# Kernel optimization log

Hardware: AMD Instinct MI355X
Metric: run time of the kernel (lower is better)

The kernel has to match this reference:

```python
import jax, jax.numpy as jnp
import numpy as np

N_NODES = 100000
N_EDGES = 1600000
IN_DIM, HID_DIM, OUT_DIM = 128, 64, 1


def setup_inputs() -> dict:
    key = jax.random.key(0)
    ks = jax.random.split(key, 8)
    x = jax.random.normal(ks[0], (N_NODES, IN_DIM), dtype=jnp.float32)
    edge_index = jax.random.randint(ks[1], (2, N_EDGES), 0, N_NODES, dtype=jnp.int64)
    # Glorot-ish scaled weights
    W1 = jax.random.normal(ks[2], (IN_DIM, HID_DIM), dtype=jnp.float32) / np.sqrt(IN_DIM)
    b1 = jnp.zeros((HID_DIM,), dtype=jnp.float32)
    W2 = jax.random.normal(ks[3], (HID_DIM, HID_DIM), dtype=jnp.float32) / np.sqrt(HID_DIM)
    b2 = jnp.zeros((HID_DIM,), dtype=jnp.float32)
    W3 = jax.random.normal(ks[4], (HID_DIM, OUT_DIM), dtype=jnp.float32) / np.sqrt(HID_DIM)
    b3 = jnp.zeros((OUT_DIM,), dtype=jnp.float32)
    return {"x": x, "edge_index": edge_index, "W1": W1, "b1": b1,
            "W2": W2, "b2": b2, "W3": W3, "b3": b3}


def _gcn_norm(edge_index, num_nodes):
    # PyG gcn_norm with add_self_loops=True, edge_weight=1:
    # deg[i] = 1 (self loop) + #incoming edges at i (dst = edge_index[1])
    dst = edge_index[1]
    deg = jnp.ones((num_nodes,), dtype=jnp.float32).at[dst].add(1.0)
    dis = jnp.where(deg > 0, 1.0 / jnp.sqrt(deg), 0.0)  # deg_inv_sqrt
    return dis


def _gcn_conv(x, W, b, src, dst, dis):
    h = x @ W                                   # [N, F_out] transform first (PyG order)
    norm = dis[src] * dis[dst]                  # [E]
    msg = h[src] * norm[:, None]                # gather + scale, [E, F_out]
    out = jnp.zeros_like(h).at[dst].add(msg)    # scatter-add aggregation
    out = out + h * (dis * dis)[:, None]        # self-loop contribution
    return out + b


def reference(x, edge_index, W1, b1, W2, b2, W3, b3):
    src, dst = edge_index[0], edge_index[1]
    dis = _gcn_norm(edge_index, x.shape[0])
    h = jax.nn.relu(_gcn_conv(x, W1, b1, src, dst, dis))   # dropout = identity (eval)
    h = jax.nn.relu(_gcn_conv(h, W2, b2, src, dst, dis))
    return _gcn_conv(h, W3, b3, src, dst, dis)
```

## Files before the change

### kernel.cpp

```cpp
#include <hip/hip_runtime.h>

#define IN_DIM 128
#define HID 64
#define MAXC 400
#define MAXB 512
#define EPB 4096
#define DPT 512
#define G1CAP 6144

static __device__ __forceinline__ unsigned short f2bf(float f) {
    unsigned u = __float_as_uint(f);
    u += 0x7FFF + ((u >> 16) & 1);
    return (unsigned short)(u >> 16);
}

typedef short bf16x8 __attribute__((ext_vector_type(8)));
typedef float f32x4 __attribute__((ext_vector_type(4)));

__global__ __launch_bounds__(256) void k_hist2(const int* __restrict__ dst,
                                               int* __restrict__ hmat, int E, int NC) {
    __shared__ int h[MAXC];
    int tid = threadIdx.x, blk = blockIdx.x;
    for (int i = tid; i < NC; i += 256) h[i] = 0;
    __syncthreads();
    int e0 = blk * EPB, e1 = min(e0 + EPB, E);
    for (int e = e0 + tid; e < e1; e += 256) atomicAdd(&h[dst[e] >> 8], 1);
    __syncthreads();
    for (int i = tid; i < NC; i += 256) hmat[blk * MAXC + i] = h[i];
}

__global__ __launch_bounds__(512) void k_bktscan(int* __restrict__ hmat,
                                                 int* __restrict__ bktTotal,
                                                 int NBLK, int NC) {
    __shared__ int tmp[512];
    int cb = blockIdx.x;
    int t = threadIdx.x;
    int v = (t < NBLK) ? hmat[t * MAXC + cb] : 0;
    tmp[t] = v;
    __syncthreads();
    for (int off = 1; off < 512; off <<= 1) {
        int a = (t >= off) ? tmp[t - off] : 0;
        __syncthreads();
        tmp[t] += a;
        __syncthreads();
    }
    if (t < NBLK) hmat[t * MAXC + cb] = tmp[t] - v;
    if (t == 511) bktTotal[cb] = tmp[511];
}

__global__ __launch_bounds__(512) void k_cscan(const int* __restrict__ bktTotal,
                                               int* __restrict__ coarseStart,
                                               int* __restrict__ rowStart,
                                               int NC, int N, int E) {
    __shared__ int tmp[512];
    int t = threadIdx.x;
    int v = (t < NC) ? bktTotal[t] : 0;
    tmp[t] = v;
    __syncthreads();
    for (int off = 1; off < 512; off <<= 1) {
        int a = (t >= off) ? tmp[t - off] : 0;
        __syncthreads();
        tmp[t] += a;
        __syncthreads();
    }
    int excl = tmp[t] - v;
    if (t < NC) coarseStart[t] = excl;
    if (t == NC - 1) coarseStart[NC] = excl + v;
    if (t == 0) rowStart[N] = E;
}

__global__ __launch_bounds__(256) void k_part1(const int* __restrict__ src,
                                               const int* __restrict__ dst,
                                               const int* __restrict__ hmat,
                                               const int* __restrict__ coarseStart,
                                               int* __restrict__ tmp1,
                                               int E, int NC) {
    __shared__ int bcnt[MAXC];
    __shared__ int bbase[MAXC];
    int tid = threadIdx.x, blk = blockIdx.x;
    for (int i = tid; i < NC; i += 256) {
        bcnt[i] = 0;
        bbase[i] = coarseStart[i] + hmat[blk * MAXC + i];
    }
    __syncthreads();
    int e0 = blk * EPB, e1 = min(e0 + EPB, E);
    for (int e = e0 + tid; e < e1; e += 256) {
        int s = src[e], d = dst[e];
        int cb = d >> 8;
        int slot = bbase[cb] + atomicAdd(&bcnt[cb], 1);
        tmp1[slot] = s | ((d & 255) << 17);
    }
}

__global__ __launch_bounds__(DPT) void k_degplace(const int* __restrict__ tmp1,
                                                  const int* __restrict__ coarseStart,
                                                  float* __restrict__ dis,
                                                  int* __restrict__ rowStart,
                                                  int* __restrict__ esrc, int N) {
    __shared__ int hist[256];
    __shared__ int scn[256];
    __shared__ int cur[256];
    int tid = threadIdx.x;
    int cb = blockIdx.x;
    int node0 = cb << 8;
    const int r0 = coarseStart[cb], r1 = coarseStart[cb + 1];
    if (tid < 256) hist[tid] = 0;
    __syncthreads();
    for (int i = r0 + tid; i < r1; i += DPT)
        atomicAdd(&hist[((unsigned)tmp1[i]) >> 17], 1);
    __syncthreads();
    int v = 0;
    if (tid < 256) { v = hist[tid]; scn[tid] = v; }
    __syncthreads();
    for (int off = 1; off < 256; off <<= 1) {
        int a = 0;
        if (tid < 256 && tid >= off) a = scn[tid - off];
        __syncthreads();
        if (tid < 256) scn[tid] += a;
        __syncthreads();
    }
    if (tid < 256) {
        int myStart = r0 + scn[tid] - v;
        cur[tid] = myStart;
        int node = node0 + tid;
        if (node < N) {
            dis[node] = rsqrtf((float)v + 1.0f);
            rowStart[node] = myStart;
        }
    }
    __syncthreads();
    for (int i = r0 + tid; i < r1; i += DPT) {
        int pk = tmp1[i];
        int dl = ((unsigned)pk) >> 17;
        int pos = atomicAdd(&cur[dl], 1);
        esrc[pos] = (pk & 0x1FFFF) << 7;
    }
}

template <int K, typename T>
__global__ __launch_bounds__(256) void k_mmx(const T* __restrict__ X,
                                             const float* __restrict__ W,
                                             const float* __restrict__ dis,
                                             unsigned short* __restrict__ Hbs, int N) {
    constexpr int WP = K + 8;
    __shared__ unsigned short Wt[64 * WP];
    const int tid = threadIdx.x;
    for (int i = tid; i < K * 64; i += 256) {
        int k = i >> 6, n = i & 63;
        Wt[n * WP + k] = f2bf(W[i]);
    }
    __syncthreads();
    const int lane = tid & 63;
    const int m16 = lane & 15;
    const int quad = lane >> 4;
    const int rowBase = blockIdx.x * 64 + (tid >> 6) * 16;
    const int rowc = min(rowBase + m16, N - 1);

    f32x4 acc0 = {0.f, 0.f, 0.f, 0.f};
    f32x4 acc1 = acc0, acc2 = acc0, acc3 = acc0;
    const T* xrow = X + (size_t)rowc * K;
#pragma unroll
    for (int k0 = 0; k0 < K; k0 += 32) {
        bf16x8 af;
        if constexpr (sizeof(T) == 4) {
            const float* xp = (const float*)xrow + k0 + quad * 8;
            float4 xa = *(const float4*)xp;
            float4 xb = *(const float4*)(xp + 4);
            af[0] = (short)f2bf(xa.x); af[1] = (short)f2bf(xa.y);
            af[2] = (short)f2bf(xa.z); af[3] = (short)f2bf(xa.w);
            af[4] = (short)f2bf(xb.x); af[5] = (short)f2bf(xb.y);
            af[6] = (short)f2bf(xb.z); af[7] = (short)f2bf(xb.w);
        } else {
            af = *(const bf16x8*)((const unsigned short*)xrow + k0 + quad * 8);
        }
        const unsigned short* wp = &Wt[m16 * WP + k0 + quad * 8];
        bf16x8 b0 = *(const bf16x8*)(wp);
        bf16x8 b1 = *(const bf16x8*)(wp + 16 * WP);
        bf16x8 b2 = *(const bf16x8*)(wp + 32 * WP);
        bf16x8 b3 = *(const bf16x8*)(wp + 48 * WP);
        acc0 = __builtin_amdgcn_mfma_f32_16x16x32_bf16(af, b0, acc0, 0, 0, 0);
        acc1 = __builtin_amdgcn_mfma_f32_16x16x32_bf16(af, b1, acc1, 0, 0, 0);
        acc2 = __builtin_amdgcn_mfma_f32_16x16x32_bf16(af, b2, acc2, 0, 0, 0);
        acc3 = __builtin_amdgcn_mfma_f32_16x16x32_bf16(af, b3, acc3, 0, 0, 0);
    }
#pragma unroll
    for (int reg = 0; reg < 4; ++reg) {
        int r = rowBase + quad * 4 + reg;
        if (r < N) {
            float dsc = dis[r];
            unsigned short* hp = Hbs + (size_t)r * 64 + m16;
            hp[0]  = f2bf(acc0[reg] * dsc);
            hp[16] = f2bf(acc1[reg] * dsc);
            hp[32] = f2bf(acc2[reg] * dsc);
            hp[48] = f2bf(acc3[reg] * dsc);
        }
    }
}


#define BLO(d) __uint_as_float((d) << 16)
#define BHI(d) __uint_as_float((d) & 0xFFFF0000u)
#define ACC4(L, H, Q) { L.x += BLO((Q).x); L.y += BHI((Q).x);                  \
                        L.z += BLO((Q).y); L.w += BHI((Q).y);                  \
                        H.x += BLO((Q).z); H.y += BHI((Q).z);                  \
                        H.z += BLO((Q).w); H.w += BHI((Q).w); }

template <int MODE>
__global__ __launch_bounds__(256) void k_gather64(const unsigned short* __restrict__ Hbs,
                                                  const int* __restrict__ esrc,
                                                  const int* __restrict__ rowStart,
                                                  const float* __restrict__ dis,
                                                  const float* __restrict__ b,
                                                  unsigned short* __restrict__ outB,
                                                  const float* __restrict__ W3,
                                                  const float* __restrict__ b3,
                                                  float* __restrict__ colS,
                                                  float* __restrict__ outF,
                                                  int N) {
    int lane = threadIdx.x & 63;
    int c = lane & 7;
    int oct = lane >> 3;
    int ob = oct << 3;
    int wave = (blockIdx.x * 256 + threadIdx.x) >> 6;
    int g0 = wave * 8;
    if (g0 >= N) return;
    const char* hb = (const char*)Hbs + c * 16;

    int rb = rowStart[min(g0 + lane, N)];
    int Rq  = __shfl(rb, oct, 64);
    int Rq1 = __shfl(rb, oct + 1, 64);
    int n = g0 + oct;
    int nc = min(n, N - 1);

    float4 aL, aH;
    {
        uint4 sd = *(const uint4*)(hb + ((size_t)nc << 7));
        aL.x = BLO(sd.x); aL.y = BHI(sd.x); aL.z = BLO(sd.y); aL.w = BHI(sd.y);
        aH.x = BLO(sd.z); aH.y = BHI(sd.z); aH.z = BLO(sd.w); aH.w = BHI(sd.w);
    }

    unsigned eoff = (Rq + c < Rq1) ? (unsigned)esrc[Rq + c] : 0u;
    for (int bb = Rq; bb < Rq1; bb += 8) {
        int cnt = min(8, Rq1 - bb);
        unsigned eoffN = (bb + 8 + c < Rq1) ? (unsigned)esrc[bb + 8 + c] : 0u;

        if (cnt == 8) {
            unsigned o0 = __shfl(eoff, ob + 0, 64);
            unsigned o1 = __shfl(eoff, ob + 1, 64);
            unsigned o2 = __shfl(eoff, ob + 2, 64);
            unsigned o3 = __shfl(eoff, ob + 3, 64);
            unsigned o4 = __shfl(eoff, ob + 4, 64);
            unsigned o5 = __shfl(eoff, ob + 5, 64);
            unsigned o6 = __shfl(eoff, ob + 6, 64);
            unsigned o7 = __shfl(eoff, ob + 7, 64);
            uint4 q0 = *(const uint4*)(hb + o0);
            uint4 q1 = *(const uint4*)(hb + o1);
            uint4 q2 = *(const uint4*)(hb + o2);
            uint4 q3 = *(const uint4*)(hb + o3);
            uint4 q4 = *(const uint4*)(hb + o4);
            uint4 q5 = *(const uint4*)(hb + o5);
            uint4 q6 = *(const uint4*)(hb + o6);
            uint4 q7 = *(const uint4*)(hb + o7);
            ACC4(aL, aH, q0) ACC4(aL, aH, q1) ACC4(aL, aH, q2) ACC4(aL, aH, q3)
            ACC4(aL, aH, q4) ACC4(aL, aH, q5) ACC4(aL, aH, q6) ACC4(aL, aH, q7)
        } else {
            int j = 0;
            if (j + 4 <= cnt) {
                unsigned o0 = __shfl(eoff, ob + j + 0, 64);
                unsigned o1 = __shfl(eoff, ob + j + 1, 64);
                unsigned o2 = __shfl(eoff, ob + j + 2, 64);
                unsigned o3 = __shfl(eoff, ob + j + 3, 64);
                uint4 q0 = *(const uint4*)(hb + o0);
                uint4 q1 = *(const uint4*)(hb + o1);
                uint4 q2 = *(const uint4*)(hb + o2);
                uint4 q3 = *(const uint4*)(hb + o3);
                ACC4(aL, aH, q0) ACC4(aL, aH, q1) ACC4(aL, aH, q2) ACC4(aL, aH, q3)
                j += 4;
            }
            if (j < cnt) {
                bool v1 = j + 1 < cnt, v2 = j + 2 < cnt;
                unsigned o0 = __shfl(eoff, ob + j, 64);
                unsigned o1 = __shfl(eoff, v1 ? ob + j + 1 : ob + j, 64);
                unsigned o2 = __shfl(eoff, v2 ? ob + j + 2 : ob + j, 64);
                uint4 q0 = *(const uint4*)(hb + o0);
                uint4 q1 = *(const uint4*)(hb + o1);
                uint4 q2 = *(const uint4*)(hb + o2);
                if (!v1) { q1.x = q1.y = q1.z = q1.w = 0u; }
                if (!v2) { q2.x = q2.y = q2.z = q2.w = 0u; }
                ACC4(aL, aH, q0) ACC4(aL, aH, q1) ACC4(aL, aH, q2)
            }
        }
        eoff = eoffN;
    }

    float ds = dis[nc];
    float4 bL = ((const float4*)b)[2 * c];
    float4 bH = ((const float4*)b)[2 * c + 1];
    float4 vL, vH;
    vL.x = fmaxf(aL.x * ds + bL.x, 0.f);
    vL.y = fmaxf(aL.y * ds + bL.y, 0.f);
    vL.z = fmaxf(aL.z * ds + bL.z, 0.f);
    vL.w = fmaxf(aL.w * ds + bL.w, 0.f);
    vH.x = fmaxf(aH.x * ds + bH.x, 0.f);
    vH.y = fmaxf(aH.y * ds + bH.y, 0.f);
    vH.z = fmaxf(aH.z * ds + bH.z, 0.f);
    vH.w = fmaxf(aH.w * ds + bH.w, 0.f);

    if (MODE == 1) {
        uint4 pv;
        pv.x = (unsigned)f2bf(vL.x) | ((unsigned)f2bf(vL.y) << 16);
        pv.y = (unsigned)f2bf(vL.z) | ((unsigned)f2bf(vL.w) << 16);
        pv.z = (unsigned)f2bf(vH.x) | ((unsigned)f2bf(vH.y) << 16);
        pv.w = (unsigned)f2bf(vH.z) | ((unsigned)f2bf(vH.w) << 16);
        if (n < N) ((uint4*)outB)[(size_t)n * 8 + c] = pv;
    } else {
        float4 wL = ((const float4*)W3)[2 * c];
        float4 wH = ((const float4*)W3)[2 * c + 1];
        float t = vL.x * wL.x + vL.y * wL.y + vL.z * wL.z + vL.w * wL.w
                + vH.x * wH.x + vH.y * wH.y + vH.z * wH.z + vH.w * wH.w;
        t += __shfl_xor(t, 1, 64);
        t += __shfl_xor(t, 2, 64);
        t += __shfl_xor(t, 4, 64);
        if (c == 0 && n < N) {
            colS[n] = t * ds;
            outF[n] = t * ds * ds + b3[0];
        }
    }
}

__global__ __launch_bounds__(256) void k_gather1(const float* __restrict__ colS,
                                                 const int* __restrict__ esrc,
                                                 const int* __restrict__ rowStart,
                                                 const float* __restrict__ dis,
                                                 float* __restrict__ out, int N) {
    __shared__ float ls[G1CAP];
    int tid = threadIdx.x;
    int n0 = blockIdx.x * 256;
    int nEnd = min(n0 + 256, N);
    int r0 = rowStart[n0];
    int r1 = rowStart[nEnd];
    int cnt = r1 - r0;
    if (cnt <= G1CAP) {
        for (int i = tid; i < cnt; i += 256)
            ls[i] = colS[((unsigned)esrc[r0 + i]) >> 7];
        __syncthreads();
        int n = n0 + tid;
        if (n < N) {
            int a = rowStart[n] - r0, bnd = rowStart[n + 1] - r0;
            float acc = 0.0f;
            for (int e = a; e < bnd; ++e) acc += ls[e];
            out[n] += acc * dis[n];
        }
    } else {
        int n = n0 + tid;
        if (n < N) {
            int a = rowStart[n], bnd = rowStart[n + 1];
            float acc = 0.0f;
            for (int e = a; e < bnd; ++e) acc += colS[((unsigned)esrc[e]) >> 7];
            out[n] += acc * dis[n];
        }
    }
}

extern "C" void kernel_launch(void* const* d_in, const int* in_sizes, int n_in,
                              void* d_out, int out_size, void* d_ws, size_t ws_size,
                              hipStream_t stream) {
    const float* x  = (const float*)d_in[0];
    const int*   ei = (const int*)d_in[1];
    const float* W1 = (const float*)d_in[2];
    const float* b1 = (const float*)d_in[3];
    const float* W2 = (const float*)d_in[4];
    const float* b2 = (const float*)d_in[5];
    const float* W3 = (const float*)d_in[6];
    const float* b3 = (const float*)d_in[7];
    float* out = (float*)d_out;

    const int N = in_sizes[0] / IN_DIM;
    const int E = in_sizes[1] / 2;
    const int* src = ei;
    const int* dst = ei + E;
    const int NC = (N + 255) >> 8;
    const int NBLK = (E + EPB - 1) / EPB;

    char* w = (char*)d_ws;
    auto alloc = [&](size_t bytes) {
        char* p = w;
        w += (bytes + 1023) & ~(size_t)1023;
        return p;
    };
    float*          dis        = (float*)alloc((size_t)N * 4);
    unsigned short* Hbs        = (unsigned short*)alloc((size_t)N * 64 * 2);
    unsigned short* Hb1        = (unsigned short*)alloc((size_t)N * 64 * 2);
    float*          colS       = (float*)alloc((size_t)N * 4);
    int*            rowStart   = (int*)alloc((size_t)(N + 1) * 4);
    int*            bktTotal   = (int*)alloc((size_t)MAXC * 4);
    int*            coarseStart= (int*)alloc((size_t)(MAXC + 1) * 4);
    int*            hmat       = (int*)alloc((size_t)MAXB * MAXC * 4);
    int*            esrc       = (int*)alloc((size_t)E * 4 + 1024);
    int*            tmp1       = (int*)alloc((size_t)E * 4);

    const int NB_N  = (N + 255) / 256;
    const int NB_MX = (N + 63) / 64;
    const int NB_G8 = (((N + 7) / 8) * 64 + 255) / 256;

    k_hist2<<<NBLK, 256, 0, stream>>>(dst, hmat, E, NC);
    k_bktscan<<<NC, 512, 0, stream>>>(hmat, bktTotal, NBLK, NC);
    k_cscan<<<1, 512, 0, stream>>>(bktTotal, coarseStart, rowStart, NC, N, E);
    k_part1<<<NBLK, 256, 0, stream>>>(src, dst, hmat, coarseStart, tmp1, E, NC);
    k_degplace<<<NC, DPT, 0, stream>>>(tmp1, coarseStart, dis, rowStart, esrc, N);

    k_mmx<IN_DIM, float><<<NB_MX, 256, 0, stream>>>(x, W1, dis, Hbs, N);
    k_gather64<1><<<NB_G8, 256, 0, stream>>>(Hbs, esrc, rowStart, dis, b1,
                                             Hb1, nullptr, nullptr, nullptr, nullptr, N);

    k_mmx<HID, unsigned short><<<NB_MX, 256, 0, stream>>>(Hb1, W2, dis, Hbs, N);
    k_gather64<2><<<NB_G8, 256, 0, stream>>>(Hbs, esrc, rowStart, dis, b2,
                                             nullptr, W3, b3, colS, out, N);

    k_gather1<<<NB_N, 256, 0, stream>>>(colS, esrc, rowStart, dis, out, N);
}
```

Baseline: 233.3 us.

## Fuse layer-1 gather with layer-2 matmul and merge scan kernels via last-block

```diff
diff --git a/kernel.cpp b/kernel.cpp
--- a/kernel.cpp
+++ b/kernel.cpp
@@ -18,9 +18,11 @@
 typedef float f32x4 __attribute__((ext_vector_type(4)));
 
 __global__ __launch_bounds__(256) void k_hist2(const int* __restrict__ dst,
-                                               int* __restrict__ hmat, int E, int NC) {
+                                               int* __restrict__ hmat,
+                                               int* __restrict__ ctr, int E, int NC) {
     __shared__ int h[MAXC];
     int tid = threadIdx.x, blk = blockIdx.x;
+    if (blk == 0 && tid == 0) ctr[0] = 0;
     for (int i = tid; i < NC; i += 256) h[i] = 0;
     __syncthreads();
     int e0 = blk * EPB, e1 = min(e0 + EPB, E);
@@ -31,8 +33,12 @@
 
 __global__ __launch_bounds__(512) void k_bktscan(int* __restrict__ hmat,
                                                  int* __restrict__ bktTotal,
-                                                 int NBLK, int NC) {
+                                                 int* __restrict__ ctr,
+                                                 int* __restrict__ coarseStart,
+                                                 int* __restrict__ rowStart,
+                                                 int NBLK, int NC, int N, int E) {
     __shared__ int tmp[512];
+    __shared__ int lastFlag;
     int cb = blockIdx.x;
     int t = threadIdx.x;
     int v = (t < NBLK) ? hmat[t * MAXC + cb] : 0;
@@ -45,17 +51,13 @@
         __syncthreads();
     }
     if (t < NBLK) hmat[t * MAXC + cb] = tmp[t] - v;
-    if (t == 511) bktTotal[cb] = tmp[511];
-}
-
-__global__ __launch_bounds__(512) void k_cscan(const int* __restrict__ bktTotal,
-                                               int* __restrict__ coarseStart,
-                                               int* __restrict__ rowStart,
-                                               int NC, int N, int E) {
-    __shared__ int tmp[512];
-    int t = threadIdx.x;
-    int v = (t < NC) ? bktTotal[t] : 0;
-    tmp[t] = v;
+    if (t == 511) atomicExch(&bktTotal[cb], tmp[511]);
+    __syncthreads();
+    if (t == 0) lastFlag = (atomicAdd(ctr, 1) == (int)gridDim.x - 1);
+    __syncthreads();
+    if (!lastFlag) return;
+    int v2 = (t < NC) ? atomicAdd(&bktTotal[t], 0) : 0;
+    tmp[t] = v2;
     __syncthreads();
     for (int off = 1; off < 512; off <<= 1) {
         int a = (t >= off) ? tmp[t - off] : 0;
@@ -63,9 +65,9 @@
         tmp[t] += a;
         __syncthreads();
     }
-    int excl = tmp[t] - v;
+    int excl = tmp[t] - v2;
     if (t < NC) coarseStart[t] = excl;
-    if (t == NC - 1) coarseStart[NC] = excl + v;
+    if (t == NC - 1) coarseStart[NC] = excl + v2;
     if (t == 0) rowStart[N] = E;
 }
 
@@ -197,7 +199,6 @@
     }
 }
 
-
 #define BLO(d) __uint_as_float((d) << 16)
 #define BHI(d) __uint_as_float((d) & 0xFFFF0000u)
 #define ACC4(L, H, Q) { L.x += BLO((Q).x); L.y += BHI((Q).x);                  \
@@ -205,13 +206,154 @@
                         H.x += BLO((Q).z); H.y += BHI((Q).z);                  \
                         H.z += BLO((Q).w); H.w += BHI((Q).w); }
 
-template <int MODE>
-__global__ __launch_bounds__(256) void k_gather64(const unsigned short* __restrict__ Hbs,
+#define GATHER_OCTET_BODY()                                                    \
+    unsigned eoff = (Rq + c < Rq1) ? (unsigned)esrc[Rq + c] : 0u;              \
+    for (int bb = Rq; bb < Rq1; bb += 8) {                                     \
+        int cnt = min(8, Rq1 - bb);                                            \
+        unsigned eoffN = (bb + 8 + c < Rq1) ? (unsigned)esrc[bb + 8 + c] : 0u; \
+        if (cnt == 8) {                                                        \
+            unsigned o0 = __shfl(eoff, ob + 0, 64);                            \
+            unsigned o1 = __shfl(eoff, ob + 1, 64);                            \
+            unsigned o2 = __shfl(eoff, ob + 2, 64);                            \
+            unsigned o3 = __shfl(eoff, ob + 3, 64);                            \
+            unsigned o4 = __shfl(eoff, ob + 4, 64);                            \
+            unsigned o5 = __shfl(eoff, ob + 5, 64);                            \
+            unsigned o6 = __shfl(eoff, ob + 6, 64);                            \
+            unsigned o7 = __shfl(eoff, ob + 7, 64);                            \
+            uint4 q0 = *(const uint4*)(hb + o0);                               \
+            uint4 q1 = *(const uint4*)(hb + o1);                               \
+            uint4 q2 = *(const uint4*)(hb + o2);                               \
+            uint4 q3 = *(const uint4*)(hb + o3);                               \
+            uint4 q4 = *(const uint4*)(hb + o4);                               \
+            uint4 q5 = *(const uint4*)(hb + o5);                               \
+            uint4 q6 = *(const uint4*)(hb + o6);                               \
+            uint4 q7 = *(const uint4*)(hb + o7);                               \
+            ACC4(aL, aH, q0) ACC4(aL, aH, q1) ACC4(aL, aH, q2) ACC4(aL, aH, q3)\
+            ACC4(aL, aH, q4) ACC4(aL, aH, q5) ACC4(aL, aH, q6) ACC4(aL, aH, q7)\
+        } else {                                                               \
+            int j = 0;                                                         \
+            if (j + 4 <= cnt) {                                                \
+                unsigned o0 = __shfl(eoff, ob + j + 0, 64);                    \
+                unsigned o1 = __shfl(eoff, ob + j + 1, 64);                    \
+                unsigned o2 = __shfl(eoff, ob + j + 2, 64);                    \
+                unsigned o3 = __shfl(eoff, ob + j + 3, 64);                    \
+                uint4 q0 = *(const uint4*)(hb + o0);                           \
+                uint4 q1 = *(const uint4*)(hb + o1);                           \
+                uint4 q2 = *(const uint4*)(hb + o2);                           \
+                uint4 q3 = *(const uint4*)(hb + o3);                           \
+                ACC4(aL, aH, q0) ACC4(aL, aH, q1)                              \
+                ACC4(aL, aH, q2) ACC4(aL, aH, q3)                              \
+                j += 4;                                                        \
+            }                                                                  \
+            if (j < cnt) {                                                     \
+                bool v1 = j + 1 < cnt, v2 = j + 2 < cnt;                       \
+                unsigned o0 = __shfl(eoff, ob + j, 64);                        \
+                unsigned o1 = __shfl(eoff, v1 ? ob + j + 1 : ob + j, 64);      \
+                unsigned o2 = __shfl(eoff, v2 ? ob + j + 2 : ob + j, 64);      \
+                uint4 q0 = *(const uint4*)(hb + o0);                           \
+                uint4 q1 = *(const uint4*)(hb + o1);                           \
+                uint4 q2 = *(const uint4*)(hb + o2);                           \
+                if (!v1) { q1.x = q1.y = q1.z = q1.w = 0u; }                   \
+                if (!v2) { q2.x = q2.y = q2.z = q2.w = 0u; }                   \
+                ACC4(aL, aH, q0) ACC4(aL, aH, q1) ACC4(aL, aH, q2)             \
+            }                                                                  \
+        }                                                                      \
+        eoff = eoffN;                                                          \
+    }
+
+__global__ __launch_bounds__(512) void k_gmx(const unsigned short* __restrict__ Hbs,
+                                             const int* __restrict__ esrc,
+                                             const int* __restrict__ rowStart,
+                                             const float* __restrict__ dis,
+                                             const float* __restrict__ b,
+                                             const float* __restrict__ W,
+                                             unsigned short* __restrict__ Hout,
+                                             int N) {
+    __shared__ unsigned short Hrow[64 * 72];
+    __shared__ unsigned short Wt[64 * 72];
+    const int tid = threadIdx.x;
+    for (int i = tid; i < 64 * 64; i += 512) {
+        int k = i >> 6, n = i & 63;
+        Wt[n * 72 + k] = f2bf(W[i]);
+    }
+    const int lane = tid & 63;
+    const int c = lane & 7;
+    const int oct = lane >> 3;
+    const int ob = oct << 3;
+    const int wv = tid >> 6;
+    const int g0 = blockIdx.x * 64 + wv * 8;
+    const char* hb = (const char*)Hbs + c * 16;
+
+    int rb = rowStart[min(g0 + lane, N)];
+    int Rq  = __shfl(rb, oct, 64);
+    int Rq1 = __shfl(rb, oct + 1, 64);
+    int n = g0 + oct;
+    int nc = min(n, N - 1);
+
+    float4 aL, aH;
+    {
+        uint4 sd = *(const uint4*)(hb + ((size_t)nc << 7));
+        aL.x = BLO(sd.x); aL.y = BHI(sd.x); aL.z = BLO(sd.y); aL.w = BHI(sd.y);
+        aH.x = BLO(sd.z); aH.y = BHI(sd.z); aH.z = BLO(sd.w); aH.w = BHI(sd.w);
+    }
+    GATHER_OCTET_BODY()
+
+    {
+        float ds = dis[nc];
+        float4 bL = ((const float4*)b)[2 * c];
+        float4 bH = ((const float4*)b)[2 * c + 1];
+        uint4 pv;
+        pv.x = (unsigned)f2bf(fmaxf(aL.x * ds + bL.x, 0.f))
+             | ((unsigned)f2bf(fmaxf(aL.y * ds + bL.y, 0.f)) << 16);
+        pv.y = (unsigned)f2bf(fmaxf(aL.z * ds + bL.z, 0.f))
+             | ((unsigned)f2bf(fmaxf(aL.w * ds + bL.w, 0.f)) << 16);
+        pv.z = (unsigned)f2bf(fmaxf(aH.x * ds + bH.x, 0.f))
+             | ((unsigned)f2bf(fmaxf(aH.y * ds + bH.y, 0.f)) << 16);
+        pv.w = (unsigned)f2bf(fmaxf(aH.z * ds + bH.z, 0.f))
+             | ((unsigned)f2bf(fmaxf(aH.w * ds + bH.w, 0.f)) << 16);
+        ((uint4*)&Hrow[(wv * 8 + oct) * 72])[c] = pv;
+    }
+    __syncthreads();
+
+    if (wv < 4) {
+        const int m16 = lane & 15;
+        const int quad = lane >> 4;
+        const int rowBase = blockIdx.x * 64 + wv * 16;
+        f32x4 acc0 = {0.f, 0.f, 0.f, 0.f};
+        f32x4 acc1 = acc0, acc2 = acc0, acc3 = acc0;
+#pragma unroll
+        for (int k0 = 0; k0 < 64; k0 += 32) {
+            bf16x8 af = *(const bf16x8*)&Hrow[(wv * 16 + m16) * 72 + k0 + quad * 8];
+            const unsigned short* wp = &Wt[m16 * 72 + k0 + quad * 8];
+            bf16x8 b0 = *(const bf16x8*)(wp);
+            bf16x8 b1 = *(const bf16x8*)(wp + 16 * 72);
+            bf16x8 b2 = *(const bf16x8*)(wp + 32 * 72);
+            bf16x8 b3 = *(const bf16x8*)(wp + 48 * 72);
+            acc0 = __builtin_amdgcn_mfma_f32_16x16x32_bf16(af, b0, acc0, 0, 0, 0);
+            acc1 = __builtin_amdgcn_mfma_f32_16x16x32_bf16(af, b1, acc1, 0, 0, 0);
+            acc2 = __builtin_amdgcn_mfma_f32_16x16x32_bf16(af, b2, acc2, 0, 0, 0);
+            acc3 = __builtin_amdgcn_mfma_f32_16x16x32_bf16(af, b3, acc3, 0, 0, 0);
+        }
+#pragma unroll
+        for (int reg = 0; reg < 4; ++reg) {
+            int r = rowBase + quad * 4 + reg;
+            if (r < N) {
+                float dsc = dis[r];
+                unsigned short* hp = Hout + (size_t)r * 64 + m16;
+                hp[0]  = f2bf(acc0[reg] * dsc);
+                hp[16] = f2bf(acc1[reg] * dsc);
+                hp[32] = f2bf(acc2[reg] * dsc);
+                hp[48] = f2bf(acc3[reg] * dsc);
+            }
+        }
+    }
+}
+
+__global__ __launch_bounds__(256) void k_gatherW3(const unsigned short* __restrict__ Hbs,
                                                   const int* __restrict__ esrc,
                                                   const int* __restrict__ rowStart,
                                                   const float* __restrict__ dis,
                                                   const float* __restrict__ b,
-                                                  unsigned short* __restrict__ outB,
                                                   const float* __restrict__ W3,
                                                   const float* __restrict__ b3,
                                                   float* __restrict__ colS,
@@ -238,60 +380,7 @@
         aL.x = BLO(sd.x); aL.y = BHI(sd.x); aL.z = BLO(sd.y); aL.w = BHI(sd.y);
         aH.x = BLO(sd.z); aH.y = BHI(sd.z); aH.z = BLO(sd.w); aH.w = BHI(sd.w);
     }
-
-    unsigned eoff = (Rq + c < Rq1) ? (unsigned)esrc[Rq + c] : 0u;
-    for (int bb = Rq; bb < Rq1; bb += 8) {
-        int cnt = min(8, Rq1 - bb);
-        unsigned eoffN = (bb + 8 + c < Rq1) ? (unsigned)esrc[bb + 8 + c] : 0u;
-
-        if (cnt == 8) {
-            unsigned o0 = __shfl(eoff, ob + 0, 64);
-            unsigned o1 = __shfl(eoff, ob + 1, 64);
-            unsigned o2 = __shfl(eoff, ob + 2, 64);
-            unsigned o3 = __shfl(eoff, ob + 3, 64);
-            unsigned o4 = __shfl(eoff, ob + 4, 64);
-            unsigned o5 = __shfl(eoff, ob + 5, 64);
-            unsigned o6 = __shfl(eoff, ob + 6, 64);
-            unsigned o7 = __shfl(eoff, ob + 7, 64);
-            uint4 q0 = *(const uint4*)(hb + o0);
-            uint4 q1 = *(const uint4*)(hb + o1);
-            uint4 q2 = *(const uint4*)(hb + o2);
-            uint4 q3 = *(const uint4*)(hb + o3);
-            uint4 q4 = *(const uint4*)(hb + o4);
-            uint4 q5 = *(const uint4*)(hb + o5);
-            uint4 q6 = *(const uint4*)(hb + o6);
-            uint4 q7 = *(const uint4*)(hb + o7);
-            ACC4(aL, aH, q0) ACC4(aL, aH, q1) ACC4(aL, aH, q2) ACC4(aL, aH, q3)
-            ACC4(aL, aH, q4) ACC4(aL, aH, q5) ACC4(aL, aH, q6) ACC4(aL, aH, q7)
-        } else {
-            int j = 0;
-            if (j + 4 <= cnt) {
-                unsigned o0 = __shfl(eoff, ob + j + 0, 64);
-                unsigned o1 = __shfl(eoff, ob + j + 1, 64);
-                unsigned o2 = __shfl(eoff, ob + j + 2, 64);
-                unsigned o3 = __shfl(eoff, ob + j + 3, 64);
-                uint4 q0 = *(const uint4*)(hb + o0);
-                uint4 q1 = *(const uint4*)(hb + o1);
-                uint4 q2 = *(const uint4*)(hb + o2);
-                uint4 q3 = *(const uint4*)(hb + o3);
-                ACC4(aL, aH, q0) ACC4(aL, aH, q1) ACC4(aL, aH, q2) ACC4(aL, aH, q3)
-                j += 4;
-            }
-            if (j < cnt) {
-                bool v1 = j + 1 < cnt, v2 = j + 2 < cnt;
-                unsigned o0 = __shfl(eoff, ob + j, 64);
-                unsigned o1 = __shfl(eoff, v1 ? ob + j + 1 : ob + j, 64);
-                unsigned o2 = __shfl(eoff, v2 ? ob + j + 2 : ob + j, 64);
-                uint4 q0 = *(const uint4*)(hb + o0);
-                uint4 q1 = *(const uint4*)(hb + o1);
-                uint4 q2 = *(const uint4*)(hb + o2);
-                if (!v1) { q1.x = q1.y = q1.z = q1.w = 0u; }
-                if (!v2) { q2.x = q2.y = q2.z = q2.w = 0u; }
-                ACC4(aL, aH, q0) ACC4(aL, aH, q1) ACC4(aL, aH, q2)
-            }
-        }
-        eoff = eoffN;
-    }
+    GATHER_OCTET_BODY()
 
     float ds = dis[nc];
     float4 bL = ((const float4*)b)[2 * c];
@@ -306,25 +395,16 @@
     vH.z = fmaxf(aH.z * ds + bH.z, 0.f);
     vH.w = fmaxf(aH.w * ds + bH.w, 0.f);
 
-    if (MODE == 1) {
-        uint4 pv;
-        pv.x = (unsigned)f2bf(vL.x) | ((unsigned)f2bf(vL.y) << 16);
-        pv.y = (unsigned)f2bf(vL.z) | ((unsigned)f2bf(vL.w) << 16);
-        pv.z = (unsigned)f2bf(vH.x) | ((unsigned)f2bf(vH.y) << 16);
-        pv.w = (unsigned)f2bf(vH.z) | ((unsigned)f2bf(vH.w) << 16);
-        if (n < N) ((uint4*)outB)[(size_t)n * 8 + c] = pv;
-    } else {
-        float4 wL = ((const float4*)W3)[2 * c];
-        float4 wH = ((const float4*)W3)[2 * c + 1];
-        float t = vL.x * wL.x + vL.y * wL.y + vL.z * wL.z + vL.w * wL.w
-                + vH.x * wH.x + vH.y * wH.y + vH.z * wH.z + vH.w * wH.w;
-        t += __shfl_xor(t, 1, 64);
-        t += __shfl_xor(t, 2, 64);
-        t += __shfl_xor(t, 4, 64);
-        if (c == 0 && n < N) {
-            colS[n] = t * ds;
-            outF[n] = t * ds * ds + b3[0];
-        }
+    float4 wL = ((const float4*)W3)[2 * c];
+    float4 wH = ((const float4*)W3)[2 * c + 1];
+    float t = vL.x * wL.x + vL.y * wL.y + vL.z * wL.z + vL.w * wL.w
+            + vH.x * wH.x + vH.y * wH.y + vH.z * wH.z + vH.w * wH.w;
+    t += __shfl_xor(t, 1, 64);
+    t += __shfl_xor(t, 2, 64);
+    t += __shfl_xor(t, 4, 64);
+    if (c == 0 && n < N) {
+        colS[n] = t * ds;
+        outF[n] = t * ds * ds + b3[0];
     }
 }
 
@@ -398,24 +478,25 @@
     int*            hmat       = (int*)alloc((size_t)MAXB * MAXC * 4);
     int*            esrc       = (int*)alloc((size_t)E * 4 + 1024);
     int*            tmp1       = (int*)alloc((size_t)E * 4);
-
-    const int NB_N  = (N + 255) / 256;
-    const int NB_MX = (N + 63) / 64;
-    const int NB_G8 = (((N + 7) / 8) * 64 + 255) / 256;
-
-    k_hist2<<<NBLK, 256, 0, stream>>>(dst, hmat, E, NC);
-    k_bktscan<<<NC, 512, 0, stream>>>(hmat, bktTotal, NBLK, NC);
-    k_cscan<<<1, 512, 0, stream>>>(bktTotal, coarseStart, rowStart, NC, N, E);
+    int*            ctr        = (int*)alloc(64);
+
+    const int NB_N   = (N + 255) / 256;
+    const int NB_MX  = (N + 63) / 64;
+    const int NB_G8  = (((N + 7) / 8) * 64 + 255) / 256;
+    const int NB_GMX = (N + 63) / 64;
+
+    k_hist2<<<NBLK, 256, 0, stream>>>(dst, hmat, ctr, E, NC);
+    k_bktscan<<<NC, 512, 0, stream>>>(hmat, bktTotal, ctr, coarseStart, rowStart,
+                                      NBLK, NC, N, E);
     k_part1<<<NBLK, 256, 0, stream>>>(src, dst, hmat, coarseStart, tmp1, E, NC);
     k_degplace<<<NC, DPT, 0, stream>>>(tmp1, coarseStart, dis, rowStart, esrc, N);
 
     k_mmx<IN_DIM, float><<<NB_MX, 256, 0, stream>>>(x, W1, dis, Hbs, N);
-    k_gather64<1><<<NB_G8, 256, 0, stream>>>(Hbs, esrc, rowStart, dis, b1,
-                                             Hb1, nullptr, nullptr, nullptr, nullptr, N);
-
-    k_mmx<HID, unsigned short><<<NB_MX, 256, 0, stream>>>(Hb1, W2, dis, Hbs, N);
-    k_gather64<2><<<NB_G8, 256, 0, stream>>>(Hbs, esrc, rowStart, dis, b2,
-                                             nullptr, W3, b3, colS, out, N);
+
+    k_gmx<<<NB_GMX, 512, 0, stream>>>(Hbs, esrc, rowStart, dis, b1, W2, Hb1, N);
+
+    k_gatherW3<<<NB_G8, 256, 0, stream>>>(Hb1, esrc, rowStart, dis, b2,
+                                          W3, b3, colS, out, N);
 
     k_gather1<<<NB_N, 256, 0, stream>>>(colS, esrc, rowStart, dis, out, N);
 }
```

Result: no change. 229.8 us (-1.5%).
